# Kernel tuning notes

Measured on AMD Instinct MI355X. Metric: run time of the kernel, lower is better.

## Reference

```python
import jax, jax.numpy as jnp
import numpy as np

BLOCK_SIZE = 3
SOBEL_PAD = 1  # sobel_size // 2
BLOCK_PAD = BLOCK_SIZE // 2

_SOBEL_X = jnp.array([[-1.0, 0.0, 1.0], [-2.0, 0.0, 2.0], [-1.0, 0.0, 1.0]], dtype=jnp.float32)[None, None]
_SOBEL_Y = jnp.array([[-1.0, -2.0, -1.0], [0.0, 0.0, 0.0], [1.0, 2.0, 1.0]], dtype=jnp.float32)[None, None]
_SUM_K = jnp.ones((1, 1, BLOCK_SIZE, BLOCK_SIZE), dtype=jnp.float32)


def _pad_replicate(x, p):
    return jnp.pad(x, ((0, 0), (0, 0), (p, p), (p, p)), mode='edge')


def _conv(x, k):
    return jax.lax.conv_general_dilated(
        x, k, window_strides=(1, 1), padding='VALID',
        dimension_numbers=('NCHW', 'OIHW', 'NCHW'))


def setup_inputs() -> dict:
    key = jax.random.key(0)
    image = jax.random.uniform(key, (8, 1, 1080, 1920), dtype=jnp.float32) * 255.0
    return {"image": image}


def reference(image) -> jnp.ndarray:
    img = image.astype(jnp.float32)
    img_p = _pad_replicate(img, SOBEL_PAD)
    Ix = _conv(img_p, _SOBEL_X)
    Iy = _conv(img_p, _SOBEL_Y)
    Ixx = Ix * Ix
    Iyy = Iy * Iy
    Ixy = Ix * Iy
    sum_Ixx = _conv(_pad_replicate(Ixx, BLOCK_PAD), _SUM_K)
    sum_Iyy = _conv(_pad_replicate(Iyy, BLOCK_PAD), _SUM_K)
    sum_Ixy = _conv(_pad_replicate(Ixy, BLOCK_PAD), _SUM_K)
    half_trace = (sum_Ixx + sum_Iyy) * 0.5
    diff_half = (sum_Ixx - sum_Iyy) * 0.5
    sqrt_disc = jnp.sqrt(diff_half * diff_half + sum_Ixy * sum_Ixy + 1e-10)
    lambda_min = half_trace - sqrt_disc
    return jnp.clip(lambda_min, 0.0)
```

## Files before the change

kernel.cpp:

```cpp
#include <hip/hip_runtime.h>

#define IMG_H 1080
#define IMG_W 1920
#define NBATCH 8
#define LSTRIP 15
#define BROWS (4*LSTRIP)
#define NK (LSTRIP+4)


template<bool EDGE>
__device__ __forceinline__ void st_body(const float* __restrict__ g,
                                        float* __restrict__ orow,
                                        int vb, int s0) {
    const bool eL = EDGE && (vb == 0);
    const bool eR = EDGE && (vb == IMG_W - 4);
    int wb = vb - 4;
    if (EDGE) { if (eL) wb = 0; if (eR) wb = IMG_W - 12; }
    const bool topFix = (s0 == 0);
    const bool botFix = (s0 + LSTRIP == IMG_H);

    float raw[5][12];
    float hdR[3][6], hsR[3][6], hfd[3], hfs[3], h[3][12];

    auto issue = [&](int k) {
        int lr = s0 - 2 + k;
        lr = max(0, min(IMG_H - 1, lr));
        const float4* rp = (const float4*)(g + (size_t)lr * IMG_W + wb);
        const float4 a = rp[0], b2 = rp[1], c = rp[2];
        float* r = raw[k % 5];
        r[0]=a.x;  r[1]=a.y;  r[2]=a.z;  r[3]=a.w;
        r[4]=b2.x; r[5]=b2.y; r[6]=b2.z; r[7]=b2.w;
        r[8]=c.x;  r[9]=c.y;  r[10]=c.z; r[11]=c.w;
    };

    #pragma unroll
    for (int k = 0; k < 4; ++k) issue(k);

    #pragma unroll
    for (int k = 0; k < NK; ++k) {
        if (k + 4 < NK) issue(k + 4);

        {
            const float* r = raw[k % 5];
            float z[8];
            if (EDGE) {
                const float zL[8] = {r[0],r[0],r[0],r[1],r[2],r[3],r[4],r[5]};
                const float zR[8] = {r[6],r[7],r[8],r[9],r[10],r[11],r[11],r[11]};
                #pragma unroll
                for (int j = 0; j < 8; ++j)
                    z[j] = eL ? zL[j] : (eR ? zR[j] : r[j + 2]);
                hfd[k % 3] = eR ? (z[5] - z[4]) : (z[3] - z[2]);
                hfs[k % 3] = eR ? (z[4] + 3.0f * z[5]) : (3.0f * z[2] + z[3]);
            } else {
                #pragma unroll
                for (int j = 0; j < 8; ++j) z[j] = r[j + 2];
            }
            float* hd = hdR[k % 3];
            float* hs = hsR[k % 3];
            #pragma unroll
            for (int t = 0; t < 6; ++t) {
                hd[t] = z[t + 2] - z[t];
                hs[t] = fmaf(2.0f, z[t + 1], z[t]) + z[t + 2];
            }
        }

        if (k >= 2) {
            const int rr = k - 2;
            const int sm = rr % 3, sz = (rr + 1) % 3, sp = (rr + 2) % 3;

            float Ix[6], Iy[6];
            #pragma unroll
            for (int t = 0; t < 6; ++t) {
                Ix[t] = hdR[sm][t] + 2.0f * hdR[sz][t] + hdR[sp][t];
                Iy[t] = hsR[sp][t] - hsR[sm][t];
            }
            if (EDGE) {
                const float ixf = hfd[sm] + 2.0f * hfd[sz] + hfd[sp];
                const float iyf = hfs[sp] - hfs[sm];
                if (eL) { Ix[0] = ixf; Iy[0] = iyf; }
                if (eR) { Ix[5] = ixf; Iy[5] = iyf; }
            }

            float pxx[6], pyy[6], pxy[6];
            #pragma unroll
            for (int t = 0; t < 6; ++t) {
                pxx[t] = Ix[t] * Ix[t];
                pyy[t] = Iy[t] * Iy[t];
                pxy[t] = Ix[t] * Iy[t];
            }
            float* hr = h[rr % 3];
            #pragma unroll
            for (int o = 0; o < 4; ++o) {
                hr[o]     = pxx[o] + pxx[o+1] + pxx[o+2];
                hr[4 + o] = pyy[o] + pyy[o+1] + pyy[o+2];
                hr[8 + o] = pxy[o] + pxy[o+1] + pxy[o+2];
            }
            if (rr == 1 && topFix) {
                #pragma unroll
                for (int q = 0; q < 12; ++q) h[0][q] = hr[q];
            }
            if (rr == LSTRIP + 1 && botFix) {
                const float* hprev = h[(rr - 1) % 3];
                #pragma unroll
                for (int q = 0; q < 12; ++q) hr[q] = hprev[q];
            }

            if (rr >= 2) {
                const float* h0 = h[(rr - 2) % 3];
                const float* h1 = h[(rr - 1) % 3];
                const float* h2 = hr;
                float rv[4];
                #pragma unroll
                for (int o = 0; o < 4; ++o) {
                    const float sxx = h0[o]     + h1[o]     + h2[o];
                    const float syy = h0[4 + o] + h1[4 + o] + h2[4 + o];
                    const float sxy = h0[8 + o] + h1[8 + o] + h2[8 + o];
                    const float ht   = 0.5f * (sxx + syy);
                    const float dh   = 0.5f * (sxx - syy);
                    const float disc = fmaf(dh, dh, fmaf(sxy, sxy, 1e-10f));
                    rv[o] = fmaxf(ht - sqrtf(disc), 0.0f);
                }
                *(float4*)orow = make_float4(rv[0], rv[1], rv[2], rv[3]);
                orow += IMG_W;
            }
        }
    }
}

__global__ __launch_bounds__(256, 3)
void shi_tomasi_kernel(const float* __restrict__ img, float* __restrict__ out) {
    const int cg    = threadIdx.x & 63;
    const int strip = threadIdx.x >> 6;
    const int vb = blockIdx.x * 256 + cg * 4;
    if (vb >= IMG_W) return;
    const int s0 = blockIdx.y * BROWS + strip * LSTRIP;
    const float* g = img + (size_t)blockIdx.z * (IMG_H * IMG_W);
    float* orow = out + ((size_t)blockIdx.z * IMG_H + s0) * IMG_W + vb;

    if (blockIdx.x == 0 || blockIdx.x == gridDim.x - 1)
        st_body<true>(g, orow, vb, s0);
    else
        st_body<false>(g, orow, vb, s0);
}

extern "C" void kernel_launch(void* const* d_in, const int* in_sizes, int n_in,
                              void* d_out, int out_size, void* d_ws, size_t ws_size,
                              hipStream_t stream) {
    const float* img = (const float*)d_in[0];
    float* out = (float*)d_out;
    dim3 grid(8, IMG_H / BROWS, NBATCH);
    shi_tomasi_kernel<<<grid, 256, 0, stream>>>(img, out);
}
```

Measured before the change: 126.9 us.

## Pack Sobel/Harris math into float2 vectors, shorten strips, nontemporal stores

Rewrites the per-thread stencil pipeline to use two-wide float vectors so the compiler can emit packed FP32 FMA/add/mul, and folds the 0.5 scaling into a single multiply after the sqrt. It shrinks each thread's row strip from 15 to 9, which gives more blocks and more parallelism but raises the share of redundant halo row loads. The load prefetch depth drops from 4 rows to 3 to save registers. Output stores now go through nontemporal stores with per-row address computation.

```diff
diff --git a/kernel.cpp b/kernel.cpp
--- a/kernel.cpp
+++ b/kernel.cpp
@@ -1,16 +1,23 @@
 #include <hip/hip_runtime.h>
+
+typedef float v2f __attribute__((ext_vector_type(2)));
+typedef float v4f __attribute__((ext_vector_type(4)));
 
 #define IMG_H 1080
 #define IMG_W 1920
 #define NBATCH 8
-#define LSTRIP 15
+#define LSTRIP 9
 #define BROWS (4*LSTRIP)
 #define NK (LSTRIP+4)
 
 
+static __device__ __forceinline__ v2f vfma2(v2f a, v2f b, v2f c) {
+    return __builtin_elementwise_fma(a, b, c);
+}
+
 template<bool EDGE>
 __device__ __forceinline__ void st_body(const float* __restrict__ g,
-                                        float* __restrict__ orow,
+                                        float* __restrict__ outb,
                                         int vb, int s0) {
     const bool eL = EDGE && (vb == 0);
     const bool eR = EDGE && (vb == IMG_W - 4);
@@ -19,109 +26,132 @@
     const bool topFix = (s0 == 0);
     const bool botFix = (s0 + LSTRIP == IMG_H);
 
-    float raw[5][12];
-    float hdR[3][6], hsR[3][6], hfd[3], hfs[3], h[3][12];
+    v2f R[4][6];
+    v2f hdR[3][3], hsR[3][3];
+    float hfd[3], hfs[3];
+    v2f hxx[3][2], hyy[3][2], hxy[3][2];
 
     auto issue = [&](int k) {
         int lr = s0 - 2 + k;
         lr = max(0, min(IMG_H - 1, lr));
         const float4* rp = (const float4*)(g + (size_t)lr * IMG_W + wb);
-        const float4 a = rp[0], b2 = rp[1], c = rp[2];
-        float* r = raw[k % 5];
-        r[0]=a.x;  r[1]=a.y;  r[2]=a.z;  r[3]=a.w;
-        r[4]=b2.x; r[5]=b2.y; r[6]=b2.z; r[7]=b2.w;
-        r[8]=c.x;  r[9]=c.y;  r[10]=c.z; r[11]=c.w;
+        const float4 A = rp[0], B = rp[1], C = rp[2];
+        v2f* r = R[k % 4];
+        r[0] = v2f{A.x, A.y}; r[1] = v2f{A.z, A.w};
+        r[2] = v2f{B.x, B.y}; r[3] = v2f{B.z, B.w};
+        r[4] = v2f{C.x, C.y}; r[5] = v2f{C.z, C.w};
     };
 
-    #pragma unroll
-    for (int k = 0; k < 4; ++k) issue(k);
+    issue(0); issue(1); issue(2);
+
+    const v2f two = {2.0f, 2.0f};
 
     #pragma unroll
     for (int k = 0; k < NK; ++k) {
-        if (k + 4 < NK) issue(k + 4);
+        if (k + 3 < NK) issue(k + 3);
 
         {
-            const float* r = raw[k % 5];
-            float z[8];
+            const v2f* r = R[k % 4];
+            v2f Za, Zb, Zc, Zd, Sab, Sbc, Scd;
             if (EDGE) {
-                const float zL[8] = {r[0],r[0],r[0],r[1],r[2],r[3],r[4],r[5]};
-                const float zR[8] = {r[6],r[7],r[8],r[9],r[10],r[11],r[11],r[11]};
+                const float rs[12] = {r[0].x, r[0].y, r[1].x, r[1].y,
+                                      r[2].x, r[2].y, r[3].x, r[3].y,
+                                      r[4].x, r[4].y, r[5].x, r[5].y};
+                const float zL[8] = {rs[0],rs[0],rs[0],rs[1],rs[2],rs[3],rs[4],rs[5]};
+                const float zR[8] = {rs[6],rs[7],rs[8],rs[9],rs[10],rs[11],rs[11],rs[11]};
+                float z[8];
                 #pragma unroll
                 for (int j = 0; j < 8; ++j)
-                    z[j] = eL ? zL[j] : (eR ? zR[j] : r[j + 2]);
+                    z[j] = eL ? zL[j] : (eR ? zR[j] : rs[j + 2]);
                 hfd[k % 3] = eR ? (z[5] - z[4]) : (z[3] - z[2]);
                 hfs[k % 3] = eR ? (z[4] + 3.0f * z[5]) : (3.0f * z[2] + z[3]);
+                Za = v2f{z[0], z[1]}; Zb = v2f{z[2], z[3]};
+                Zc = v2f{z[4], z[5]}; Zd = v2f{z[6], z[7]};
+                Sab = v2f{z[1], z[2]}; Sbc = v2f{z[3], z[4]}; Scd = v2f{z[5], z[6]};
             } else {
-                #pragma unroll
-                for (int j = 0; j < 8; ++j) z[j] = r[j + 2];
+                Za = r[1]; Zb = r[2]; Zc = r[3]; Zd = r[4];
+                Sab = v2f{r[1].y, r[2].x};
+                Sbc = v2f{r[2].y, r[3].x};
+                Scd = v2f{r[3].y, r[4].x};
             }
-            float* hd = hdR[k % 3];
-            float* hs = hsR[k % 3];
-            #pragma unroll
-            for (int t = 0; t < 6; ++t) {
-                hd[t] = z[t + 2] - z[t];
-                hs[t] = fmaf(2.0f, z[t + 1], z[t]) + z[t + 2];
-            }
+            v2f* hd = hdR[k % 3];
+            v2f* hs = hsR[k % 3];
+            hd[0] = Zb - Za; hd[1] = Zc - Zb; hd[2] = Zd - Zc;
+            hs[0] = vfma2(Sab, two, Za) + Zb;
+            hs[1] = vfma2(Sbc, two, Zb) + Zc;
+            hs[2] = vfma2(Scd, two, Zc) + Zd;
         }
 
         if (k >= 2) {
             const int rr = k - 2;
             const int sm = rr % 3, sz = (rr + 1) % 3, sp = (rr + 2) % 3;
 
-            float Ix[6], Iy[6];
+            v2f Ixp[3], Iyp[3];
             #pragma unroll
-            for (int t = 0; t < 6; ++t) {
-                Ix[t] = hdR[sm][t] + 2.0f * hdR[sz][t] + hdR[sp][t];
-                Iy[t] = hsR[sp][t] - hsR[sm][t];
+            for (int j = 0; j < 3; ++j) {
+                Ixp[j] = vfma2(hdR[sz][j], two, hdR[sm][j]) + hdR[sp][j];
+                Iyp[j] = hsR[sp][j] - hsR[sm][j];
             }
             if (EDGE) {
                 const float ixf = hfd[sm] + 2.0f * hfd[sz] + hfd[sp];
                 const float iyf = hfs[sp] - hfs[sm];
-                if (eL) { Ix[0] = ixf; Iy[0] = iyf; }
-                if (eR) { Ix[5] = ixf; Iy[5] = iyf; }
+                if (eL) { Ixp[0].x = ixf; Iyp[0].x = iyf; }
+                if (eR) { Ixp[2].y = ixf; Iyp[2].y = iyf; }
             }
 
-            float pxx[6], pyy[6], pxy[6];
+            v2f xx[3], yy[3], xy[3];
             #pragma unroll
-            for (int t = 0; t < 6; ++t) {
-                pxx[t] = Ix[t] * Ix[t];
-                pyy[t] = Iy[t] * Iy[t];
-                pxy[t] = Ix[t] * Iy[t];
+            for (int j = 0; j < 3; ++j) {
+                xx[j] = Ixp[j] * Ixp[j];
+                yy[j] = Iyp[j] * Iyp[j];
+                xy[j] = Ixp[j] * Iyp[j];
             }
-            float* hr = h[rr % 3];
-            #pragma unroll
-            for (int o = 0; o < 4; ++o) {
-                hr[o]     = pxx[o] + pxx[o+1] + pxx[o+2];
-                hr[4 + o] = pyy[o] + pyy[o+1] + pyy[o+2];
-                hr[8 + o] = pxy[o] + pxy[o+1] + pxy[o+2];
+            {
+                v2f* hx = hxx[rr % 3];
+                v2f* hy = hyy[rr % 3];
+                v2f* hz = hxy[rr % 3];
+                hx[0] = xx[0] + v2f{xx[0].y, xx[1].x} + xx[1];
+                hx[1] = xx[1] + v2f{xx[1].y, xx[2].x} + xx[2];
+                hy[0] = yy[0] + v2f{yy[0].y, yy[1].x} + yy[1];
+                hy[1] = yy[1] + v2f{yy[1].y, yy[2].x} + yy[2];
+                hz[0] = xy[0] + v2f{xy[0].y, xy[1].x} + xy[1];
+                hz[1] = xy[1] + v2f{xy[1].y, xy[2].x} + xy[2];
             }
             if (rr == 1 && topFix) {
                 #pragma unroll
-                for (int q = 0; q < 12; ++q) h[0][q] = hr[q];
+                for (int q = 0; q < 2; ++q) {
+                    hxx[0][q] = hxx[1][q]; hyy[0][q] = hyy[1][q]; hxy[0][q] = hxy[1][q];
+                }
             }
             if (rr == LSTRIP + 1 && botFix) {
-                const float* hprev = h[(rr - 1) % 3];
                 #pragma unroll
-                for (int q = 0; q < 12; ++q) hr[q] = hprev[q];
+                for (int q = 0; q < 2; ++q) {
+                    hxx[rr % 3][q] = hxx[(rr - 1) % 3][q];
+                    hyy[rr % 3][q] = hyy[(rr - 1) % 3][q];
+                    hxy[rr % 3][q] = hxy[(rr - 1) % 3][q];
+                }
             }
 
             if (rr >= 2) {
-                const float* h0 = h[(rr - 2) % 3];
-                const float* h1 = h[(rr - 1) % 3];
-                const float* h2 = hr;
+                const int a = (rr - 2) % 3, b2 = (rr - 1) % 3, c = rr % 3;
                 float rv[4];
                 #pragma unroll
-                for (int o = 0; o < 4; ++o) {
-                    const float sxx = h0[o]     + h1[o]     + h2[o];
-                    const float syy = h0[4 + o] + h1[4 + o] + h2[4 + o];
-                    const float sxy = h0[8 + o] + h1[8 + o] + h2[8 + o];
-                    const float ht   = 0.5f * (sxx + syy);
-                    const float dh   = 0.5f * (sxx - syy);
-                    const float disc = fmaf(dh, dh, fmaf(sxy, sxy, 1e-10f));
-                    rv[o] = fmaxf(ht - sqrtf(disc), 0.0f);
+                for (int q = 0; q < 2; ++q) {
+                    const v2f sxx = hxx[a][q] + hxx[b2][q] + hxx[c][q];
+                    const v2f syy = hyy[a][q] + hyy[b2][q] + hyy[c][q];
+                    const v2f sxy = hxy[a][q] + hxy[b2][q] + hxy[c][q];
+                    const v2f S = sxx + syy;
+                    const v2f D = sxx - syy;
+                    const v2f E = sxy + sxy;
+                    const v2f disc = vfma2(D, D, vfma2(E, E, v2f{4e-10f, 4e-10f}));
+                    const v2f qv = {__builtin_sqrtf(disc.x), __builtin_sqrtf(disc.y)};
+                    const v2f lam = (S - qv) * 0.5f;
+                    rv[2 * q]     = fmaxf(lam.x, 0.0f);
+                    rv[2 * q + 1] = fmaxf(lam.y, 0.0f);
                 }
-                *(float4*)orow = make_float4(rv[0], rv[1], rv[2], rv[3]);
-                orow += IMG_W;
+                float* orowp = outb + (size_t)(s0 + rr - 2) * IMG_W + vb;
+                __builtin_nontemporal_store(v4f{rv[0], rv[1], rv[2], rv[3]},
+                                            (v4f*)orowp);
             }
         }
     }
@@ -135,12 +165,12 @@
     if (vb >= IMG_W) return;
     const int s0 = blockIdx.y * BROWS + strip * LSTRIP;
     const float* g = img + (size_t)blockIdx.z * (IMG_H * IMG_W);
-    float* orow = out + ((size_t)blockIdx.z * IMG_H + s0) * IMG_W + vb;
+    float* outb = out + (size_t)blockIdx.z * (IMG_H * IMG_W);
 
     if (blockIdx.x == 0 || blockIdx.x == gridDim.x - 1)
-        st_body<true>(g, orow, vb, s0);
+        st_body<true>(g, outb, vb, s0);
     else
-        st_body<false>(g, orow, vb, s0);
+        st_body<false>(g, outb, vb, s0);
 }
 
 extern "C" void kernel_launch(void* const* d_in, const int* in_sizes, int n_in,
```

Measured after the change: 121.9 us. 3.9% less time.
